# Kernel optimization log

Measured on AMD Instinct MI355X. Metric: run time of the kernel, lower is better.

## Reference

```python
import jax, jax.numpy as jnp
import numpy as np
import math

NUM_HEADS = 16

def get_slopes(n):
    def pow2(n):
        start = 2 ** (-2 ** (-(math.log2(n) - 3)))
        return [start * start ** i for i in range(n)]
    if math.log2(n).is_integer():
        return pow2(n)
    c = 2 ** math.floor(math.log2(n))
    return pow2(c) + get_slopes(2 * c)[0::2][: n - c]


def setup_inputs() -> dict:
    key = jax.random.key(0)
    ks = jax.random.split(key, 5)
    B, T, C = 2, 2048, 1024
    return {
        "x": jax.random.normal(ks[0], (B, T, C), dtype=jnp.float32),
        "W_qkv": jax.random.normal(ks[1], (C, 3 * C), dtype=jnp.float32) * 0.02,
        "b_qkv": jax.random.normal(ks[2], (3 * C,), dtype=jnp.float32) * 0.02,
        "W_proj": jax.random.normal(ks[3], (C, C), dtype=jnp.float32) * 0.02,
        "b_proj": jax.random.normal(ks[4], (C,), dtype=jnp.float32) * 0.02,
    }


def reference(x, W_qkv, b_qkv, W_proj, b_proj):
    B, T, C = x.shape
    H = NUM_HEADS
    D = C // H
    qkv = x @ W_qkv + b_qkv                       # [B,T,3C]
    q, k, v = jnp.split(qkv, 3, axis=-1)
    q = q.reshape(B, T, H, D).transpose(0, 2, 1, 3)  # [B,H,T,D]
    k = k.reshape(B, T, H, D).transpose(0, 2, 1, 3)
    v = v.reshape(B, T, H, D).transpose(0, 2, 1, 3)

    slopes = jnp.asarray(get_slopes(H), dtype=jnp.float32)  # [H]
    idx = jnp.arange(T)
    # alibi_bias(L).T in source: -(i-j) for j<=i, 0 for j>i  == min(j-i, 0)
    alibi = jnp.minimum(idx[None, :] - idx[:, None], 0).astype(jnp.float32)  # [T,T]
    bias = slopes[:, None, None] * alibi          # [H,T,T]

    scale = 1.0 / math.sqrt(D)
    scores = jnp.einsum("bhtd,bhsd->bhts", q, k) * scale + bias[None]
    # NOTE: source code builds a causal -inf mask but never adds it -> non-causal
    w = jax.nn.softmax(scores, axis=-1)
    y = jnp.einsum("bhts,bhsd->bhtd", w, v)       # [B,H,T,D]
    y = y.transpose(0, 2, 1, 3).reshape(B, T, C)
    return y @ W_proj + b_proj
```

## Files before the change

### kernel.cpp

```cpp
#include <hip/hip_runtime.h>
#include <hip/hip_bf16.h>
#include <cmath>
#include <cstdint>

typedef __bf16 bf16_t;
typedef __bf16 bf16x8 __attribute__((ext_vector_type(8)));
typedef float f32x4 __attribute__((ext_vector_type(4)));
typedef float f32x8 __attribute__((ext_vector_type(8)));

static_assert(sizeof(bf16x8) == 16, "bf16x8 must be 16B");

#define MFMA16(a, b, c) __builtin_amdgcn_mfma_f32_16x16x32_bf16((a), (b), (c), 0, 0, 0)

__device__ __forceinline__ void load_lds_16B(const bf16_t* gsrc, bf16_t* ldst) {
  __builtin_amdgcn_global_load_lds(
      (const __attribute__((address_space(1))) void*)gsrc,
      (__attribute__((address_space(3))) void*)ldst, 16, 0, 0);
}

__global__ void detect_dtype(const unsigned short* __restrict__ x,
                             int* __restrict__ flag) {
  const int lane = threadIdx.x;
  int cnt = 0;
#pragma unroll
  for (int t = 0; t < 8; ++t) {
    unsigned short u = x[2 * (lane + 64 * t)];
    int e = (u >> 7) & 0xFF;
    cnt += (e >= 90 && e <= 130) ? 1 : 0;
  }
#pragma unroll
  for (int off = 1; off < 64; off <<= 1) cnt += __shfl_xor(cnt, off, 64);
  if (lane == 0) *flag = (cnt < 300) ? 1 : 0;
}

__global__ __launch_bounds__(256) void convert_x(const void* __restrict__ x_,
                                                 bf16_t* __restrict__ xb,
                                                 const int* __restrict__ flagp) {
  const size_t idx = ((size_t)blockIdx.x * 256 + threadIdx.x) * 8;
  if (*flagp) {
    f32x8 v = *(const f32x8*)((const float*)x_ + idx);
    bf16x8 bv;
#pragma unroll
    for (int e = 0; e < 8; ++e) bv[e] = (bf16_t)v[e];
    *(bf16x8*)&xb[idx] = bv;
  } else {
    *(bf16x8*)&xb[idx] = *(const bf16x8*)((const bf16_t*)x_ + idx);
  }
}

__global__ __launch_bounds__(256) void wt_transpose(const void* __restrict__ W_,
                                                    bf16_t* __restrict__ Wt,
                                                    int K, int N,
                                                    const int* __restrict__ flagp) {
  __shared__ bf16_t tile[64 * 72];
  const int is_f32 = *flagp;
  const int tid = threadIdx.x;
  const int k0 = blockIdx.y * 64;
  const int n0 = blockIdx.x * 64;
  const int r = tid >> 3;
  const int c = (tid & 7) * 8;
#pragma unroll
  for (int t = 0; t < 2; ++t) {
    int rr = r + t * 32;
    if (is_f32) {
      const float* W = (const float*)W_;
      f32x8 v = *(const f32x8*)&W[(size_t)(k0 + rr) * N + n0 + c];
      bf16x8 bv;
#pragma unroll
      for (int e = 0; e < 8; ++e) bv[e] = (bf16_t)v[e];
      *(bf16x8*)&tile[rr * 72 + c] = bv;
    } else {
      const bf16_t* W = (const bf16_t*)W_;
      *(bf16x8*)&tile[rr * 72 + c] = *(const bf16x8*)&W[(size_t)(k0 + rr) * N + n0 + c];
    }
  }
  __syncthreads();
#pragma unroll
  for (int t = 0; t < 2; ++t) {
    int rr = r + t * 32;
    bf16x8 v;
#pragma unroll
    for (int e = 0; e < 8; ++e) v[e] = tile[(c + e) * 72 + rr];
    *(bf16x8*)&Wt[(size_t)(n0 + rr) * K + k0 + c] = v;
  }
}

__global__ __launch_bounds__(256, 2) void gemm_bt(
    const bf16_t* __restrict__ A, const bf16_t* __restrict__ Bt,
    const void* __restrict__ bias_, void* __restrict__ C_,
    bf16_t* __restrict__ qb, bf16_t* __restrict__ kb, bf16_t* __restrict__ vt,
    int M, int N, int K, int mode, const int* __restrict__ flagp) {
  __shared__ bf16_t As[128 * 64];
  __shared__ bf16_t Bs[128 * 64];
  const int is_f32 = *flagp;
  const int tid = threadIdx.x;
  const int wave = tid >> 6, lane = tid & 63;
  const int l16 = lane & 15, quad = lane >> 4;
  const int m0 = blockIdx.y * 128, n0 = blockIdx.x * 128;
  const int wm = (wave >> 1) * 64, wn = (wave & 1) * 64;
  const int lr = lane >> 3, lc = (lane & 7) * 8;
  f32x4 acc[4][4] = {};

  for (int k0 = 0; k0 < K; k0 += 64) {
#pragma unroll
    for (int t = 0; t < 4; ++t) {
      const int chunk = wave * 4 + t;
      const int row = chunk * 8 + lr;
      load_lds_16B(&A[(size_t)(m0 + row) * K + k0 + lc], &As[chunk * 512]);
      load_lds_16B(&Bt[(size_t)(n0 + row) * K + k0 + lc], &Bs[chunk * 512]);
    }
    __syncthreads();
#pragma unroll
    for (int ks = 0; ks < 2; ++ks) {
      bf16x8 af[4], bfr[4];
#pragma unroll
      for (int i = 0; i < 4; ++i) {
        af[i]  = *(const bf16x8*)&As[(wm + i * 16 + l16) * 64 + ks * 32 + quad * 8];
        bfr[i] = *(const bf16x8*)&Bs[(wn + i * 16 + l16) * 64 + ks * 32 + quad * 8];
      }
#pragma unroll
      for (int i = 0; i < 4; ++i)
#pragma unroll
        for (int j = 0; j < 4; ++j)
          acc[i][j] = MFMA16(af[i], bfr[j], acc[i][j]);
    }
    __syncthreads();
  }

#pragma unroll
  for (int j = 0; j < 4; ++j) {
    const int n = n0 + wn + j * 16 + l16;
    const float bv = is_f32 ? ((const float*)bias_)[n]
                            : (float)((const bf16_t*)bias_)[n];
    if (mode == 0) {
#pragma unroll
      for (int i = 0; i < 4; ++i)
#pragma unroll
        for (int r = 0; r < 4; ++r) {
          int m = m0 + wm + i * 16 + quad * 4 + r;
          float val = acc[i][j][r] + bv;
          if (is_f32) ((float*)C_)[(size_t)m * N + n] = val;
          else ((bf16_t*)C_)[(size_t)m * N + n] = (bf16_t)val;
        }
    } else {
      const int region = n >> 10;
      const int nn = n & 1023;
      const int hh = nn >> 6, dd = nn & 63;
#pragma unroll
      for (int i = 0; i < 4; ++i)
#pragma unroll
        for (int r = 0; r < 4; ++r) {
          int m = m0 + wm + i * 16 + quad * 4 + r;
          int bb = m >> 11, tt = m & 2047;
          size_t bh = (size_t)(bb * 16 + hh);
          float val = acc[i][j][r] + bv;
          if (region == 0)
            qb[(bh * 2048 + tt) * 64 + dd] = (bf16_t)val;
          else if (region == 1)
            kb[(bh * 2048 + tt) * 64 + dd] = (bf16_t)val;
          else
            vt[bh * 131072 + (size_t)dd * 2048 + tt] = (bf16_t)val;
        }
    }
  }
}

__global__ __launch_bounds__(512, 4) void attn_kernel(
    const bf16_t* __restrict__ qbuf, const bf16_t* __restrict__ kbuf,
    const bf16_t* __restrict__ vT, bf16_t* __restrict__ y) {
  const int T = 2048;
  __shared__ __align__(16) char smem[57344];
  bf16_t* Ks  = (bf16_t*)smem;
  bf16_t* VTs = (bf16_t*)(smem + 18432);
  bf16_t* Ps  = (bf16_t*)(smem + 36864);

  const int tid = threadIdx.x;
  const int wave = tid >> 6, lane = tid & 63;
  const int g2 = wave >> 2, wp = wave & 3;
  const int l16 = lane & 15, quad = lane >> 4;
  const int bh = blockIdx.y;
  const int b = bh >> 4, h = bh & 15;
  const int i0 = blockIdx.x * 128 + wp * 32;
  const float L2E = 1.44269504088896f;
  const float c1 = 0.125f * L2E;
  const float c2 = exp2f(-0.5f * (float)(h + 1)) * L2E;

  bf16x8 qf[2][2];
#pragma unroll
  for (int g = 0; g < 2; ++g) {
    const bf16_t* qrow = qbuf + ((size_t)bh * T + i0 + g * 16 + l16) * 64;
    qf[g][0] = *(const bf16x8*)&qrow[quad * 8];
    qf[g][1] = *(const bf16x8*)&qrow[32 + quad * 8];
  }

  f32x4 o[2][4] = {};
  float rsum[2][4] = {};

  const bf16_t* kbase = kbuf + (size_t)bh * T * 64;
  const bf16_t* vbase = vT + (size_t)bh * 64 * T;

  bf16_t* myKs = Ks + g2 * 4608;
  bf16_t* myVs = VTs + g2 * 4608;
  bf16_t* Pw = Ps + wave * 1280;

  const int gtid = tid & 255;
  const int sr = gtid >> 3, sc = (gtid & 7) * 8;
  const int jbase = g2 * 1024;

  for (int jj = 0; jj < 1024; jj += 64) {
    const int j0 = jbase + jj;
#pragma unroll
    for (int t = 0; t < 2; ++t) {
      int rr = sr + t * 32;
      *(bf16x8*)&myKs[rr * 72 + sc] = *(const bf16x8*)&kbase[(size_t)(j0 + rr) * 64 + sc];
      *(bf16x8*)&myVs[rr * 72 + sc] = *(const bf16x8*)&vbase[(size_t)rr * T + j0 + sc];
    }
    __syncthreads();

#pragma unroll
    for (int hl = 0; hl < 2; ++hl) {
      bf16x8 kf[2][2];
#pragma unroll
      for (int jtl = 0; jtl < 2; ++jtl) {
        const int jr = (hl * 2 + jtl) * 16 + l16;
        kf[jtl][0] = *(const bf16x8*)&myKs[jr * 72 + quad * 8];
        kf[jtl][1] = *(const bf16x8*)&myKs[jr * 72 + 32 + quad * 8];
      }
#pragma unroll
      for (int g = 0; g < 2; ++g) {
        f32x4 s[2] = {};
#pragma unroll
        for (int jtl = 0; jtl < 2; ++jtl) {
          s[jtl] = MFMA16(qf[g][0], kf[jtl][0], s[jtl]);
          s[jtl] = MFMA16(qf[g][1], kf[jtl][1], s[jtl]);
        }
        const float fb = (float)(i0 + g * 16 + quad * 4);
#pragma unroll
        for (int jtl = 0; jtl < 2; ++jtl) {
          const float jmf = (float)(j0 + (hl * 2 + jtl) * 16 + l16);
#pragma unroll
          for (int r = 0; r < 4; ++r) {
            float dm = fminf(jmf - (fb + (float)r), 0.0f);
            float p = exp2f(c1 * s[jtl][r] + c2 * dm);
            rsum[g][r] += p;
            Pw[(g * 16 + quad * 4 + r) * 40 + jtl * 16 + l16] = (bf16_t)p;
          }
        }
      }
      __asm__ volatile("s_waitcnt lgkmcnt(0)" ::: "memory");

      bf16x8 vf[4];
#pragma unroll
      for (int dt = 0; dt < 4; ++dt)
        vf[dt] = *(const bf16x8*)&myVs[(dt * 16 + l16) * 72 + hl * 32 + quad * 8];
#pragma unroll
      for (int g = 0; g < 2; ++g) {
        const bf16x8 pf = *(const bf16x8*)&Pw[(g * 16 + l16) * 40 + quad * 8];
#pragma unroll
        for (int dt = 0; dt < 4; ++dt)
          o[g][dt] = MFMA16(pf, vf[dt], o[g][dt]);
      }
    }
    __syncthreads();
  }

#pragma unroll
  for (int g = 0; g < 2; ++g)
#pragma unroll
    for (int r = 0; r < 4; ++r) {
      float s = rsum[g][r];
      s += __shfl_xor(s, 1, 64);
      s += __shfl_xor(s, 2, 64);
      s += __shfl_xor(s, 4, 64);
      s += __shfl_xor(s, 8, 64);
      rsum[g][r] = s;
    }

  __syncthreads();
  float* exO = (float*)smem;
  float* exR = (float*)(smem + 36864);
  if (g2 == 1) {
    float* myO = exO + wp * (32 * 65);
#pragma unroll
    for (int g = 0; g < 2; ++g)
#pragma unroll
      for (int dt = 0; dt < 4; ++dt)
#pragma unroll
        for (int r = 0; r < 4; ++r)
          myO[(g * 16 + quad * 4 + r) * 65 + dt * 16 + l16] = o[g][dt][r];
    if (l16 == 0) {
#pragma unroll
      for (int g = 0; g < 2; ++g)
#pragma unroll
        for (int r = 0; r < 4; ++r)
          exR[wp * 32 + g * 16 + quad * 4 + r] = rsum[g][r];
    }
  }
  __syncthreads();
  if (g2 == 0) {
    float* myO = exO + wp * (32 * 65);
#pragma unroll
    for (int g = 0; g < 2; ++g)
#pragma unroll
      for (int dt = 0; dt < 4; ++dt)
#pragma unroll
        for (int r = 0; r < 4; ++r) {
          const int row = g * 16 + quad * 4 + r;
          const float denom = rsum[g][r] + exR[wp * 32 + row];
          const float val = (o[g][dt][r] + myO[row * 65 + dt * 16 + l16]) / denom;
          const int ig = i0 + row;
          const int d = dt * 16 + l16;
          y[((size_t)(b * 2048 + ig)) * 1024 + h * 64 + d] = (bf16_t)val;
        }
  }
}

extern "C" void kernel_launch(void* const* d_in, const int* in_sizes, int n_in,
                              void* d_out, int out_size, void* d_ws, size_t ws_size,
                              hipStream_t stream) {
  const void* x     = d_in[0];
  const void* Wqkv  = d_in[1];
  const void* bqkv  = d_in[2];
  const void* Wproj = d_in[3];
  const void* bproj = d_in[4];

  const size_t SEG = (size_t)32 * 2048 * 64;
  bf16_t* ws = (bf16_t*)d_ws;
  bf16_t* qb = ws;
  bf16_t* kb = ws + SEG;
  bf16_t* vt = ws + 2 * SEG;
  bf16_t* yb = ws + 3 * SEG;
  bf16_t* WqkvT  = yb;
  bf16_t* WprojT = qb;
  bf16_t* xb = (bf16_t*)d_out;
  int* flag1 = (int*)((char*)d_ws + (size_t)31 * 1024 * 1024);
  int* flag2 = (int*)((char*)d_ws + (size_t)4 * 1024 * 1024);

  detect_dtype<<<1, 64, 0, stream>>>((const unsigned short*)x, flag1);
  wt_transpose<<<dim3(48, 16), 256, 0, stream>>>(Wqkv, WqkvT, 1024, 3072, flag1);
  convert_x<<<2048, 256, 0, stream>>>(x, xb, flag1);
  gemm_bt<<<dim3(24, 32), 256, 0, stream>>>(xb, WqkvT, bqkv, nullptr, qb, kb, vt,
                                            4096, 3072, 1024, 1, flag1);
  attn_kernel<<<dim3(16, 32), 512, 0, stream>>>(qb, kb, vt, yb);
  detect_dtype<<<1, 64, 0, stream>>>((const unsigned short*)x, flag2);
  wt_transpose<<<dim3(16, 16), 256, 0, stream>>>(Wproj, WprojT, 1024, 1024, flag2);
  gemm_bt<<<dim3(8, 32), 256, 0, stream>>>(yb, WprojT, bproj, d_out,
                                           nullptr, nullptr, nullptr,
                                           4096, 1024, 1024, 0, flag2);
}
```

Measured before the change: 250.6 us.

## Stage V-transpose epilogue through LDS and specialize ALiBi softmax by tile region

In the QKV GEMM, V-region tiles are now transposed through a padded shared-memory buffer and written to the V^T buffer with 16-byte vector stores, replacing scattered 2-byte strided stores. In attention, the per-wave P scratch is halved by processing one 16-row group at a time, shrinking LDS so the occupancy hint rises from 4 to 6 blocks. The ALiBi bias path is split into branches for fully-above-diagonal tiles (no bias), fully-below tiles (linear bias with no min), and diagonal tiles. V fragment loads are hoisted ahead of the score MFMAs. The trade-offs are more register pressure from the higher occupancy target and more frequent LDS waits per group.

```diff
diff --git a/kernel.cpp b/kernel.cpp
--- a/kernel.cpp
+++ b/kernel.cpp
@@ -90,8 +90,11 @@
     const void* __restrict__ bias_, void* __restrict__ C_,
     bf16_t* __restrict__ qb, bf16_t* __restrict__ kb, bf16_t* __restrict__ vt,
     int M, int N, int K, int mode, const int* __restrict__ flagp) {
-  __shared__ bf16_t As[128 * 64];
-  __shared__ bf16_t Bs[128 * 64];
+  __shared__ __align__(16) char smem[34816];
+  bf16_t* As = (bf16_t*)smem;
+  bf16_t* Bs = As + 128 * 64;
+  bf16_t* VT = (bf16_t*)smem;
+
   const int is_f32 = *flagp;
   const int tid = threadIdx.x;
   const int wave = tid >> 6, lane = tid & 63;
@@ -127,6 +130,35 @@
     __syncthreads();
   }
 
+  const int region = (mode == 1) ? (n0 >> 10) : -1;
+
+  if (mode == 1 && region == 2) {
+#pragma unroll
+    for (int j = 0; j < 4; ++j) {
+      const int nl = wn + j * 16 + l16;
+      const float bv = is_f32 ? ((const float*)bias_)[n0 + nl]
+                              : (float)((const bf16_t*)bias_)[n0 + nl];
+#pragma unroll
+      for (int i = 0; i < 4; ++i)
+#pragma unroll
+        for (int r = 0; r < 4; ++r)
+          VT[nl * 136 + wm + i * 16 + quad * 4 + r] = (bf16_t)(acc[i][j][r] + bv);
+    }
+    __syncthreads();
+    const int bb = m0 >> 11, t0 = m0 & 2047;
+#pragma unroll
+    for (int p = 0; p < 8; ++p) {
+      const int row = p * 16 + (tid >> 4);
+      const int ms = (tid & 15) * 8;
+      const int nn = (n0 + row) & 1023;
+      const size_t bh = (size_t)(bb * 16 + (nn >> 6));
+      const int dd = nn & 63;
+      *(bf16x8*)&vt[bh * 131072 + (size_t)dd * 2048 + t0 + ms] =
+          *(const bf16x8*)&VT[row * 136 + ms];
+    }
+    return;
+  }
+
 #pragma unroll
   for (int j = 0; j < 4; ++j) {
     const int n = n0 + wn + j * 16 + l16;
@@ -143,7 +175,6 @@
           else ((bf16_t*)C_)[(size_t)m * N + n] = (bf16_t)val;
         }
     } else {
-      const int region = n >> 10;
       const int nn = n & 1023;
       const int hh = nn >> 6, dd = nn & 63;
 #pragma unroll
@@ -156,20 +187,18 @@
           float val = acc[i][j][r] + bv;
           if (region == 0)
             qb[(bh * 2048 + tt) * 64 + dd] = (bf16_t)val;
-          else if (region == 1)
+          else
             kb[(bh * 2048 + tt) * 64 + dd] = (bf16_t)val;
-          else
-            vt[bh * 131072 + (size_t)dd * 2048 + tt] = (bf16_t)val;
         }
     }
   }
 }
 
-__global__ __launch_bounds__(512, 4) void attn_kernel(
+__global__ __launch_bounds__(512, 6) void attn_kernel(
     const bf16_t* __restrict__ qbuf, const bf16_t* __restrict__ kbuf,
     const bf16_t* __restrict__ vT, bf16_t* __restrict__ y) {
   const int T = 2048;
-  __shared__ __align__(16) char smem[57344];
+  __shared__ __align__(16) char smem[47104];
   bf16_t* Ks  = (bf16_t*)smem;
   bf16_t* VTs = (bf16_t*)(smem + 18432);
   bf16_t* Ps  = (bf16_t*)(smem + 36864);
@@ -201,7 +230,7 @@
 
   bf16_t* myKs = Ks + g2 * 4608;
   bf16_t* myVs = VTs + g2 * 4608;
-  bf16_t* Pw = Ps + wave * 1280;
+  bf16_t* Pw = Ps + wave * 640;
 
   const int gtid = tid & 255;
   const int sr = gtid >> 3, sc = (gtid & 7) * 8;
@@ -226,6 +255,12 @@
         kf[jtl][0] = *(const bf16x8*)&myKs[jr * 72 + quad * 8];
         kf[jtl][1] = *(const bf16x8*)&myKs[jr * 72 + 32 + quad * 8];
       }
+      bf16x8 vf[4];
+#pragma unroll
+      for (int dt = 0; dt < 4; ++dt)
+        vf[dt] = *(const bf16x8*)&myVs[(dt * 16 + l16) * 72 + hl * 32 + quad * 8];
+
+      const int klo = j0 + hl * 32;
 #pragma unroll
       for (int g = 0; g < 2; ++g) {
         f32x4 s[2] = {};
@@ -234,28 +269,44 @@
           s[jtl] = MFMA16(qf[g][0], kf[jtl][0], s[jtl]);
           s[jtl] = MFMA16(qf[g][1], kf[jtl][1], s[jtl]);
         }
-        const float fb = (float)(i0 + g * 16 + quad * 4);
-#pragma unroll
-        for (int jtl = 0; jtl < 2; ++jtl) {
-          const float jmf = (float)(j0 + (hl * 2 + jtl) * 16 + l16);
-#pragma unroll
-          for (int r = 0; r < 4; ++r) {
-            float dm = fminf(jmf - (fb + (float)r), 0.0f);
-            float p = exp2f(c1 * s[jtl][r] + c2 * dm);
-            rsum[g][r] += p;
-            Pw[(g * 16 + quad * 4 + r) * 40 + jtl * 16 + l16] = (bf16_t)p;
+        const int rlo = i0 + g * 16;
+        if (klo >= rlo + 15) {
+#pragma unroll
+          for (int jtl = 0; jtl < 2; ++jtl)
+#pragma unroll
+            for (int r = 0; r < 4; ++r) {
+              float p = exp2f(c1 * s[jtl][r]);
+              rsum[g][r] += p;
+              Pw[(quad * 4 + r) * 40 + jtl * 16 + l16] = (bf16_t)p;
+            }
+        } else if (klo + 31 < rlo) {
+#pragma unroll
+          for (int jtl = 0; jtl < 2; ++jtl) {
+            const float base =
+                c2 * (float)((klo + jtl * 16 + l16) - (rlo + quad * 4));
+#pragma unroll
+            for (int r = 0; r < 4; ++r) {
+              float p = exp2f(c1 * s[jtl][r] + (base - c2 * (float)r));
+              rsum[g][r] += p;
+              Pw[(quad * 4 + r) * 40 + jtl * 16 + l16] = (bf16_t)p;
+            }
+          }
+        } else {
+          const float fb = (float)(rlo + quad * 4);
+#pragma unroll
+          for (int jtl = 0; jtl < 2; ++jtl) {
+            const float jmf = (float)(klo + jtl * 16 + l16);
+#pragma unroll
+            for (int r = 0; r < 4; ++r) {
+              float dm = fminf(jmf - (fb + (float)r), 0.0f);
+              float p = exp2f(c1 * s[jtl][r] + c2 * dm);
+              rsum[g][r] += p;
+              Pw[(quad * 4 + r) * 40 + jtl * 16 + l16] = (bf16_t)p;
+            }
           }
         }
-      }
-      __asm__ volatile("s_waitcnt lgkmcnt(0)" ::: "memory");
-
-      bf16x8 vf[4];
-#pragma unroll
-      for (int dt = 0; dt < 4; ++dt)
-        vf[dt] = *(const bf16x8*)&myVs[(dt * 16 + l16) * 72 + hl * 32 + quad * 8];
-#pragma unroll
-      for (int g = 0; g < 2; ++g) {
-        const bf16x8 pf = *(const bf16x8*)&Pw[(g * 16 + l16) * 40 + quad * 8];
+        __asm__ volatile("s_waitcnt lgkmcnt(0)" ::: "memory");
+        const bf16x8 pf = *(const bf16x8*)&Pw[l16 * 40 + quad * 8];
 #pragma unroll
         for (int dt = 0; dt < 4; ++dt)
           o[g][dt] = MFMA16(pf, vf[dt], o[g][dt]);
```

Result: slower. 624.5 us (+149.2%).
